# Kernel tuning notes

Hardware: AMD Instinct MI355X
Metric: run time of the kernel (lower is better)

Reference implementation:

```python
import jax, jax.numpy as jnp
import numpy as np

B = 32768
H = 320          # pred_hidden
V = 34           # num_classes
BLANK = V - 1    # padding_idx for embedding


def setup_inputs() -> dict:
    key = jax.random.key(0)
    ks = jax.random.split(key, 12)
    s = 0.05
    embed_W = jax.random.normal(ks[0], (V, H), jnp.float32) * s
    embed_W = embed_W.at[BLANK].set(0.0)  # padding_idx row is zeros in torch
    return {
        "x": jax.random.randint(ks[1], (B,), 0, V, jnp.int32),
        "enc_proj_line": jax.random.normal(ks[2], (B, H), jnp.float32),
        "h": jax.random.normal(ks[3], (1, B, H), jnp.float32),
        "c": jax.random.normal(ks[4], (1, B, H), jnp.float32),
        "embed_W": embed_W,
        "W_ih": jax.random.normal(ks[5], (4 * H, H), jnp.float32) * s,
        "W_hh": jax.random.normal(ks[6], (4 * H, H), jnp.float32) * s,
        "b_ih": jax.random.normal(ks[7], (4 * H,), jnp.float32) * s,
        "b_hh": jax.random.normal(ks[8], (4 * H,), jnp.float32) * s,
        "pred_W": jax.random.normal(ks[9], (H, H), jnp.float32) * s,
        "pred_b": jnp.zeros((H,), jnp.float32),
        "joint_W": jax.random.normal(ks[10], (V, H), jnp.float32) * s,
        "joint_b": jnp.zeros((V,), jnp.float32),
    }


def reference(x, enc_proj_line, h, c, embed_W, W_ih, W_hh, b_ih, b_hh,
              pred_W, pred_b, joint_W, joint_b):
    # embedding lookup: [B, H]
    emb = embed_W[x]
    # single-timestep LSTM cell (torch gate order: i, f, g, o)
    gates = emb @ W_ih.T + b_ih + h[0] @ W_hh.T + b_hh  # [B, 4H]
    i, f, g, o = jnp.split(gates, 4, axis=-1)
    i = jax.nn.sigmoid(i)
    f = jax.nn.sigmoid(f)
    g = jnp.tanh(g)
    o = jax.nn.sigmoid(o)
    c_new = f * c[0] + i * g                 # [B, H]
    h_new = o * jnp.tanh(c_new)              # [B, H] == g[0] (lstm output)
    # pred projection + joint
    pred_proj = h_new @ pred_W.T + pred_b    # [B, H]
    joint_out = (enc_proj_line + pred_proj) @ joint_W.T + joint_b  # [B, V]
    dec = jnp.argmax(joint_out, axis=-1)
    return dec, h_new[None], c_new[None]
```

## Files before the change

### kernel.cpp

```cpp
#include <hip/hip_runtime.h>
#include <math.h>

#define NB 32768
#define H 320
#define V 34
#define N4 1280
#define BM 128
#define BN 128
#define KSTEPS 10
#define NWIN 5
#define NWG ((NB / BM) * (N4 / BN))

typedef _Float16 f16;
typedef f16 f16x4 __attribute__((ext_vector_type(4)));
typedef f16 f16x8 __attribute__((ext_vector_type(8)));
typedef float f32x4 __attribute__((ext_vector_type(4)));

#define WS_GTP 0
#define WS_JB2 54400
#define WS_B_BYTE 217744
#define BT_COUNT (N4 * H)
#define WS_JP_BYTE 1856144
#define JP_COUNT (48 * 640)
#define WS_AT_BYTE 1979136
#define AT_COUNT (NB * H)

#define JBM 64
#define JBK 32
#define JKSTEPS 20

#define PREP_P4 1280
#define PREP_P2 50
#define PREP_P0 170
#define PREP_P3 120
#define PREP_NWG (PREP_P4 + PREP_P2 + PREP_P0 + PREP_P3 + 1)

__device__ __forceinline__ float sigf(float x) {
    return 1.0f / (1.0f + __expf(-x));
}
__device__ __forceinline__ float tanh_fast(float x) {
    return 1.0f - 2.0f / (1.0f + __expf(2.0f * x));
}

typedef const __attribute__((address_space(1))) unsigned int* gas_t;
typedef __attribute__((address_space(3))) unsigned int* las_t;

__device__ __forceinline__ void split8(const float* e, f16x8& p1, f16x8& p2) {
    #pragma unroll
    for (int j = 0; j < 8; ++j) {
        f16 a = (f16)e[j];
        p1[j] = a;
        p2[j] = (f16)((e[j] - (float)a) * 2048.0f);
    }
}

__device__ __forceinline__ void split8_res(const float* e, f16x8& p1, f16x8& p2) {
    #pragma unroll
    for (int j = 0; j < 8; ++j) {
        f16 a = (f16)e[j];
        p1[j] = a;
        p2[j] = (f16)(e[j] - (float)a);
    }
}

__global__ void prep(const float* __restrict__ embed_W,
                     const float* __restrict__ W_ih,
                     const float* __restrict__ b_ih,
                     const float* __restrict__ b_hh,
                     const float* __restrict__ pred_W,
                     const float* __restrict__ pred_b,
                     const float* __restrict__ joint_W,
                     const float* __restrict__ joint_b,
                     const float* __restrict__ W_hh,
                     const float* __restrict__ h_in,
                     float* __restrict__ ws) {
    const int bid = blockIdx.x;
    const int t = threadIdx.x;
    if (bid < PREP_P4) {
        int id = bid * 256 + t;
        int ks = id >> 15, m = id & 32767;
        const float* src = h_in + (size_t)m * H + ks * 32;
        f16* at1 = (f16*)((char*)ws + WS_AT_BYTE);
        f16* at2 = at1 + AT_COUNT;
        size_t tbase = ((size_t)(m >> 7) * KSTEPS + ks) * 4096
                       + ((m & 127) >> 4) * 512 + (m & 15) * 8;
        #pragma unroll
        for (int g = 0; g < 4; ++g) {
            float4 v0 = *(const float4*)(src + g * 8);
            float4 v1 = *(const float4*)(src + g * 8 + 4);
            float e[8] = {v0.x, v0.y, v0.z, v0.w, v1.x, v1.y, v1.z, v1.w};
            f16x8 p1, p2;
            split8_res(e, p1, p2);
            *(f16x8*)(at1 + tbase + g * 128) = p1;
            *(f16x8*)(at2 + tbase + g * 128) = p2;
        }
    } else if (bid < PREP_P4 + PREP_P2) {
        int id = (bid - PREP_P4) * 256 + t;
        int ks = id / 1280, n = id - ks * 1280;
        int orig = (n & 3) * H + (n >> 2);
        const float* src = W_hh + (size_t)orig * H + ks * 32;
        f16* bt1 = (f16*)((char*)ws + WS_B_BYTE);
        f16* bt2 = bt1 + BT_COUNT;
        size_t tbase = ((size_t)(n >> 7) * KSTEPS + ks) * 4096
                       + ((n & 127) >> 4) * 512 + (n & 15) * 8;
        #pragma unroll
        for (int g = 0; g < 4; ++g) {
            float4 v0 = *(const float4*)(src + g * 8);
            float4 v1 = *(const float4*)(src + g * 8 + 4);
            float e[8] = {v0.x, v0.y, v0.z, v0.w, v1.x, v1.y, v1.z, v1.w};
            f16x8 p1, p2;
            split8(e, p1, p2);
            *(f16x8*)(bt1 + tbase + g * 128) = p1;
            *(f16x8*)(bt2 + tbase + g * 128) = p2;
        }
    } else if (bid < PREP_P4 + PREP_P2 + PREP_P0) {
        int id = (bid - PREP_P4 - PREP_P2) * 256 + t;
        int v = id / N4, n = id % N4;
        int orig = (n & 3) * H + (n >> 2);
        float acc = b_ih[orig] + b_hh[orig];
        const float* e = embed_W + (size_t)v * H;
        const float* w = W_ih + (size_t)orig * H;
        for (int k = 0; k < H; k += 4) {
            float4 e4 = *(const float4*)(e + k);
            float4 w4 = *(const float4*)(w + k);
            acc = fmaf(e4.x, w4.x, acc);
            acc = fmaf(e4.y, w4.y, acc);
            acc = fmaf(e4.z, w4.z, acc);
            acc = fmaf(e4.w, w4.w, acc);
        }
        ws[WS_GTP + id] = acc;
    } else if (bid < PREP_P4 + PREP_P2 + PREP_P0 + PREP_P3) {
        int id = (bid - PREP_P4 - PREP_P2 - PREP_P0) * 256 + t;
        int n = id / 640, k = id % 640;
        float wv = 0.0f;
        if (n < V) {
            if (k < H) {
                wv = joint_W[(size_t)n * H + k];
            } else {
                float acc = 0.0f;
                const float* jw = joint_W + (size_t)n * H;
                for (int j = 0; j < H; ++j)
                    acc = fmaf(jw[j], pred_W[(size_t)j * H + (k - H)], acc);
                wv = acc;
            }
        }
        f16 w1 = (f16)wv;
        f16 w2 = (f16)((wv - (float)w1) * 2048.0f);
        int kk = k & 31;
        int off = (k >> 5) * 1536 + (n >> 4) * 512 + (kk >> 3) * 128
                  + (n & 15) * 8 + (kk & 7);
        f16* jp1 = (f16*)((char*)ws + WS_JP_BYTE);
        jp1[off] = w1;
        jp1[JP_COUNT + off] = w2;
    } else {
        if (t < V) {
            float acc = joint_b[t];
            const float* jw = joint_W + (size_t)t * H;
            for (int j = 0; j < H; ++j)
                acc = fmaf(jw[j], pred_b[j], acc);
            ws[WS_JB2 + t] = acc;
        }
    }
}

__launch_bounds__(256, 2)
__global__ void lstm_gemm_fast(const int* __restrict__ x,
                               const float* __restrict__ c_in,
                               const float* __restrict__ ws,
                               float* __restrict__ out) {
    __shared__ __align__(16) char smem[65536];
    const int tid = threadIdx.x, lane = tid & 63, w = tid >> 6;

    int l = (blockIdx.x & 7) * (NWG / 8) + (blockIdx.x >> 3);
    const int mb = l / (N4 / BN);
    const int nb = l % (N4 / BN);
    const int m0 = mb * BM, n0 = nb * BN;

    const f16* At1 = (const f16*)((const char*)ws + WS_AT_BYTE);
    const f16* At2 = At1 + AT_COUNT;
    const f16* Bt1 = (const f16*)((const char*)ws + WS_B_BYTE);
    const f16* Bt2 = Bt1 + BT_COUNT;
    const float* gtp = ws + WS_GTP;
    float* hn_out = out + NB;
    float* cn_out = out + NB + (size_t)NB * H;

    const int asub = (w >> 1) * 4;
    const int bsub = (w & 1) * 4;
    const int lo = lane * 8;

    auto stageB = [&](int T, int parity) {
        const f16* srcp = (w < 2) ? Bt1 : Bt2;
        const int p = (w < 2) ? 0 : 1;
        #pragma unroll
        for (int ksl = 0; ksl < 2; ++ksl) {
            const f16* src = srcp + (size_t)(nb * KSTEPS + 2 * T + ksl) * 4096
                             + (w & 1) * 2048;
            char* dst = smem + parity * 32768 + p * 16384 + ksl * 8192
                        + (w & 1) * 4096;
            #pragma unroll
            for (int i = 0; i < 4; ++i) {
                __builtin_amdgcn_global_load_lds(
                    (gas_t)(const void*)(src + i * 512 + lane * 8),
                    (las_t)(void*)(dst + i * 1024), 16, 0, 0);
            }
        }
    };

    f32x4 acc[4][4];
    #pragma unroll
    for (int i = 0; i < 4; ++i)
        #pragma unroll
        for (int j = 0; j < 4; ++j)
            acc[i][j] = (f32x4){0.f, 0.f, 0.f, 0.f};

    stageB(0, 0);
    __syncthreads();

    const int hk0 = n0 >> 2;
    float cpre[16];
    #pragma unroll
    for (int it = 0; it < 16; ++it)
        cpre[it] = c_in[(size_t)(m0 + it * 8 + (tid >> 5)) * H + hk0 + (tid & 31)];

    #pragma unroll
    for (int T = 0; T < NWIN; ++T) {
        const int par = T & 1;
        const f16* B1 = (const f16*)(smem + par * 32768);
        const f16* B2 = B1 + 8192;

        f16x8 b1a[4], b2a[4];
        #pragma unroll
        for (int nj = 0; nj < 4; ++nj) {
            b1a[nj] = *(const f16x8*)(B1 + (bsub + nj) * 512 + lo);
            b2a[nj] = *(const f16x8*)(B2 + (bsub + nj) * 512 + lo);
        }
        f16x8 a1a[4], a2a[4];
        {
            const f16* a1b = At1 + (size_t)(mb * KSTEPS + 2 * T) * 4096;
            const f16* a2b = At2 + (size_t)(mb * KSTEPS + 2 * T) * 4096;
            #pragma unroll
            for (int mi = 0; mi < 4; ++mi) {
                a1a[mi] = *(const f16x8*)(a1b + (asub + mi) * 512 + lo);
                a2a[mi] = *(const f16x8*)(a2b + (asub + mi) * 512 + lo);
            }
        }
        if (T < NWIN - 1) stageB(T + 1, par ^ 1);

        __builtin_amdgcn_s_setprio(1);
        #pragma unroll
        for (int mi = 0; mi < 4; ++mi)
            #pragma unroll
            for (int nj = 0; nj < 4; ++nj)
                acc[mi][nj] = __builtin_amdgcn_mfma_f32_16x16x32_f16(
                    a1a[mi], b1a[nj], acc[mi][nj], 0, 0, 0);
        __builtin_amdgcn_s_setprio(0);
        #pragma unroll
        for (int mi = 0; mi < 4; ++mi)
            #pragma unroll
            for (int j = 0; j < 8; ++j)
                a1a[mi][j] = a1a[mi][j] * (f16)0.00048828125f;
        __builtin_amdgcn_s_setprio(1);
        #pragma unroll
        for (int mi = 0; mi < 4; ++mi)
            #pragma unroll
            for (int nj = 0; nj < 4; ++nj)
                acc[mi][nj] = __builtin_amdgcn_mfma_f32_16x16x32_f16(
                    a1a[mi], b2a[nj], acc[mi][nj], 0, 0, 0);
        __builtin_amdgcn_s_setprio(0);

        f16x8 a1c[4], a2c[4];
        {
            const f16* a1b = At1 + (size_t)(mb * KSTEPS + 2 * T + 1) * 4096;
            const f16* a2b = At2 + (size_t)(mb * KSTEPS + 2 * T + 1) * 4096;
            #pragma unroll
            for (int mi = 0; mi < 4; ++mi) {
                a1c[mi] = *(const f16x8*)(a1b + (asub + mi) * 512 + lo);
                a2c[mi] = *(const f16x8*)(a2b + (asub + mi) * 512 + lo);
            }
        }

        __builtin_amdgcn_s_setprio(1);
        #pragma unroll
        for (int mi = 0; mi < 4; ++mi)
            #pragma unroll
            for (int nj = 0; nj < 4; ++nj)
                acc[mi][nj] = __builtin_amdgcn_mfma_f32_16x16x32_f16(
                    a2a[mi], b1a[nj], acc[mi][nj], 0, 0, 0);
        __builtin_amdgcn_s_setprio(0);

        f16x8 b1c[4], b2c[4];
        #pragma unroll
        for (int nj = 0; nj < 4; ++nj) {
            b1c[nj] = *(const f16x8*)(B1 + 4096 + (bsub + nj) * 512 + lo);
            b2c[nj] = *(const f16x8*)(B2 + 4096 + (bsub + nj) * 512 + lo);
        }
        __builtin_amdgcn_s_setprio(1);
        #pragma unroll
        for (int mi = 0; mi < 4; ++mi)
            #pragma unroll
            for (int nj = 0; nj < 4; ++nj)
                acc[mi][nj] = __builtin_amdgcn_mfma_f32_16x16x32_f16(
                    a1c[mi], b1c[nj], acc[mi][nj], 0, 0, 0);
        __builtin_amdgcn_s_setprio(0);
        #pragma unroll
        for (int mi = 0; mi < 4; ++mi)
            #pragma unroll
            for (int j = 0; j < 8; ++j)
                a1c[mi][j] = a1c[mi][j] * (f16)0.00048828125f;
        __builtin_amdgcn_s_setprio(1);
        #pragma unroll
        for (int mi = 0; mi < 4; ++mi)
            #pragma unroll
            for (int nj = 0; nj < 4; ++nj)
                acc[mi][nj] = __builtin_amdgcn_mfma_f32_16x16x32_f16(
                    a1c[mi], b2c[nj], acc[mi][nj], 0, 0, 0);
        #pragma unroll
        for (int mi = 0; mi < 4; ++mi)
            #pragma unroll
            for (int nj = 0; nj < 4; ++nj)
                acc[mi][nj] = __builtin_amdgcn_mfma_f32_16x16x32_f16(
                    a2c[mi], b1c[nj], acc[mi][nj], 0, 0, 0);
        __builtin_amdgcn_s_setprio(0);

        __syncthreads();
    }

    const int wm = (w >> 1) * 64, wn = (w & 1) * 64;
    float* gates = (float*)smem;
    #pragma unroll
    for (int mi = 0; mi < 4; ++mi)
        #pragma unroll
        for (int nj = 0; nj < 4; ++nj) {
            f32x4 v = acc[mi][nj];
            int n = wn + nj * 16 + (lane & 15);
            int r0 = wm + mi * 16 + (lane >> 4) * 4;
            #pragma unroll
            for (int q = 0; q < 4; ++q) {
                int row = r0 + q;
                gates[row * 128 + (n ^ ((row & 7) << 2))] = v[q];
            }
        }
    __syncthreads();

    #pragma unroll
    for (int it = 0; it < 16; ++it) {
        int ml = it * 8 + (tid >> 5), hkl = tid & 31;
        int k0s = (ml & 7) << 2;
        f32x4 g4 = *(const f32x4*)&gates[ml * 128 + ((hkl * 4) ^ k0s)];
        int m = m0 + ml;
        int hk = hk0 + hkl;
        int xv = x[m];
        float4 b4 = *(const float4*)(gtp + (size_t)xv * N4 + n0 + hkl * 4);
        float ig = sigf(g4[0] + b4.x);
        float fg = sigf(g4[1] + b4.y);
        float gg = tanh_fast(g4[2] + b4.z);
        float og = sigf(g4[3] + b4.w);
        float cn = fmaf(fg, cpre[it], ig * gg);
        float hn = og * tanh_fast(cn);
        hn_out[(size_t)m * H + hk] = hn;
        cn_out[(size_t)m * H + hk] = cn;
    }
}

__launch_bounds__(256, 2)
__global__ void joint_argmax(const float* __restrict__ enc,
                             const float* __restrict__ ws,
                             float* __restrict__ out) {
    __shared__ __align__(16) char smem[28672];
    const int tid = threadIdx.x, lane = tid & 63, w = tid >> 6;
    const int m0 = blockIdx.x * JBM;

    const f16* Jp1 = (const f16*)((const char*)ws + WS_JP_BYTE);
    const f16* Jp2 = Jp1 + JP_COUNT;
    const float* hn = out + NB;
    const float* jb2 = ws + WS_JB2;

    f16* base = (f16*)smem;

    f32x4 accM[3], accC[3];
    #pragma unroll
    for (int j = 0; j < 3; ++j) {
        accM[j] = (f32x4){0.f, 0.f, 0.f, 0.f};
        accC[j] = (f32x4){0.f, 0.f, 0.f, 0.f};
    }

    auto stage = [&](int t, f16* A1, f16* A2, f16* B1, f16* B2) {
        const float* srcp = (t < 10) ? enc : hn;
        const int koff = (t % 10) * JBK;
        int row = (tid >> 6) * 16 + (tid & 15);
        int k0 = ((tid & 63) >> 4) * 8;
        const float* sp = srcp + (size_t)(m0 + row) * H + koff + k0;
        float4 v0 = *(const float4*)sp;
        float4 v1 = *(const float4*)(sp + 4);
        float e[8] = {v0.x, v0.y, v0.z, v0.w, v1.x, v1.y, v1.z, v1.w};
        f16x8 p1, p2;
        split8(e, p1, p2);
        *(f16x8*)(A1 + tid * 8) = p1;
        *(f16x8*)(A2 + tid * 8) = p2;
        if (tid < 192) {
            *(int4*)(B1 + tid * 8) = *(const int4*)(Jp1 + t * 1536 + tid * 8);
            *(int4*)(B2 + tid * 8) = *(const int4*)(Jp2 + t * 1536 + tid * 8);
        }
    };

    stage(0, base, base + 2048, base + 4096, base + 5632);
    __syncthreads();

    const int lo = lane * 8;
    int cur = 0;
    for (int t = 0; t < JKSTEPS; ++t) {
        if (t < JKSTEPS - 1) {
            f16* nb_ = base + (cur ^ 1) * 7168;
            stage(t + 1, nb_, nb_ + 2048, nb_ + 4096, nb_ + 5632);
        }
        f16* A1 = base + cur * 7168;
        f16* A2 = A1 + 2048;
        f16* B1 = A1 + 4096;
        f16* B2 = A1 + 5632;

        f16x8 a1 = *(const f16x8*)(A1 + w * 512 + lo);
        f16x8 a2 = *(const f16x8*)(A2 + w * 512 + lo);
        f16x8 b1[3], b2[3];
        #pragma unroll
        for (int nj = 0; nj < 3; ++nj) {
            b1[nj] = *(const f16x8*)(B1 + nj * 512 + lo);
            b2[nj] = *(const f16x8*)(B2 + nj * 512 + lo);
        }
        #pragma unroll
        for (int nj = 0; nj < 3; ++nj) {
            accM[nj] = __builtin_amdgcn_mfma_f32_16x16x32_f16(a1, b1[nj], accM[nj], 0, 0, 0);
            accC[nj] = __builtin_amdgcn_mfma_f32_16x16x32_f16(a1, b2[nj], accC[nj], 0, 0, 0);
            accC[nj] = __builtin_amdgcn_mfma_f32_16x16x32_f16(a2, b1[nj], accC[nj], 0, 0, 0);
        }
        __syncthreads();
        cur ^= 1;
    }

    float* lg = (float*)smem;
    const int wm = w * 16;
    #pragma unroll
    for (int nj = 0; nj < 3; ++nj) {
        int n = nj * 16 + (lane & 15);
        int mr = wm + (lane >> 4) * 4;
        #pragma unroll
        for (int q = 0; q < 4; ++q)
            lg[(mr + q) * 49 + n] = fmaf(accC[nj][q], 1.0f / 2048.0f, accM[nj][q]);
    }
    __syncthreads();

    if (tid < JBM) {
        const float* row = lg + tid * 49;
        float best = row[0] + jb2[0];
        int bi = 0;
        #pragma unroll
        for (int v = 1; v < V; ++v) {
            float t2 = row[v] + jb2[v];
            if (t2 > best) { best = t2; bi = v; }
        }
        out[m0 + tid] = (float)bi;
    }
}

extern "C" void kernel_launch(void* const* d_in, const int* in_sizes, int n_in,
                              void* d_out, int out_size, void* d_ws, size_t ws_size,
                              hipStream_t stream) {
    const int*   x       = (const int*)  d_in[0];
    const float* enc     = (const float*)d_in[1];
    const float* h       = (const float*)d_in[2];
    const float* c       = (const float*)d_in[3];
    const float* embed_W = (const float*)d_in[4];
    const float* W_ih    = (const float*)d_in[5];
    const float* W_hh    = (const float*)d_in[6];
    const float* b_ih    = (const float*)d_in[7];
    const float* b_hh    = (const float*)d_in[8];
    const float* pred_W  = (const float*)d_in[9];
    const float* pred_b  = (const float*)d_in[10];
    const float* joint_W = (const float*)d_in[11];
    const float* joint_b = (const float*)d_in[12];
    float* out = (float*)d_out;
    float* ws  = (float*)d_ws;

    prep<<<PREP_NWG, 256, 0, stream>>>(embed_W, W_ih, b_ih, b_hh,
                                       pred_W, pred_b, joint_W, joint_b,
                                       W_hh, h, ws);
    lstm_gemm_fast<<<NWG, 256, 0, stream>>>(x, c, ws, out);
    joint_argmax<<<NB / JBM, 256, 0, stream>>>(enc, ws, out);
}
```

Baseline: 159.6 us.

## Fuse h fp16 split conversion into LSTM GEMM, drop prep tiling pass

Removes the prep stage that converted the fp32 hidden state into two tiled fp16 hi/lo arrays in workspace. The GEMM kernel now loads fp32 h rows directly and performs the hi/lo split in registers right before the MFMAs. This removes a large workspace write and readback. In exchange, conversion is repeated per N-block and the loads are less coalesced than the pre-tiled layout.

```diff
diff --git a/kernel.cpp b/kernel.cpp
--- a/kernel.cpp
+++ b/kernel.cpp
@@ -22,18 +22,15 @@
 #define BT_COUNT (N4 * H)
 #define WS_JP_BYTE 1856144
 #define JP_COUNT (48 * 640)
-#define WS_AT_BYTE 1979136
-#define AT_COUNT (NB * H)
 
 #define JBM 64
 #define JBK 32
 #define JKSTEPS 20
 
-#define PREP_P4 1280
 #define PREP_P2 50
 #define PREP_P0 170
 #define PREP_P3 120
-#define PREP_NWG (PREP_P4 + PREP_P2 + PREP_P0 + PREP_P3 + 1)
+#define PREP_NWG (PREP_P2 + PREP_P0 + PREP_P3 + 1)
 
 __device__ __forceinline__ float sigf(float x) {
     return 1.0f / (1.0f + __expf(-x));
@@ -54,7 +51,9 @@
     }
 }
 
-__device__ __forceinline__ void split8_res(const float* e, f16x8& p1, f16x8& p2) {
+__device__ __forceinline__ void cvt_split(const float4& v0, const float4& v1,
+                                          f16x8& p1, f16x8& p2) {
+    float e[8] = {v0.x, v0.y, v0.z, v0.w, v1.x, v1.y, v1.z, v1.w};
     #pragma unroll
     for (int j = 0; j < 8; ++j) {
         f16 a = (f16)e[j];
@@ -72,30 +71,11 @@
                      const float* __restrict__ joint_W,
                      const float* __restrict__ joint_b,
                      const float* __restrict__ W_hh,
-                     const float* __restrict__ h_in,
                      float* __restrict__ ws) {
     const int bid = blockIdx.x;
     const int t = threadIdx.x;
-    if (bid < PREP_P4) {
+    if (bid < PREP_P2) {
         int id = bid * 256 + t;
-        int ks = id >> 15, m = id & 32767;
-        const float* src = h_in + (size_t)m * H + ks * 32;
-        f16* at1 = (f16*)((char*)ws + WS_AT_BYTE);
-        f16* at2 = at1 + AT_COUNT;
-        size_t tbase = ((size_t)(m >> 7) * KSTEPS + ks) * 4096
-                       + ((m & 127) >> 4) * 512 + (m & 15) * 8;
-        #pragma unroll
-        for (int g = 0; g < 4; ++g) {
-            float4 v0 = *(const float4*)(src + g * 8);
-            float4 v1 = *(const float4*)(src + g * 8 + 4);
-            float e[8] = {v0.x, v0.y, v0.z, v0.w, v1.x, v1.y, v1.z, v1.w};
-            f16x8 p1, p2;
-            split8_res(e, p1, p2);
-            *(f16x8*)(at1 + tbase + g * 128) = p1;
-            *(f16x8*)(at2 + tbase + g * 128) = p2;
-        }
-    } else if (bid < PREP_P4 + PREP_P2) {
-        int id = (bid - PREP_P4) * 256 + t;
         int ks = id / 1280, n = id - ks * 1280;
         int orig = (n & 3) * H + (n >> 2);
         const float* src = W_hh + (size_t)orig * H + ks * 32;
@@ -113,8 +93,8 @@
             *(f16x8*)(bt1 + tbase + g * 128) = p1;
             *(f16x8*)(bt2 + tbase + g * 128) = p2;
         }
-    } else if (bid < PREP_P4 + PREP_P2 + PREP_P0) {
-        int id = (bid - PREP_P4 - PREP_P2) * 256 + t;
+    } else if (bid < PREP_P2 + PREP_P0) {
+        int id = (bid - PREP_P2) * 256 + t;
         int v = id / N4, n = id % N4;
         int orig = (n & 3) * H + (n >> 2);
         float acc = b_ih[orig] + b_hh[orig];
@@ -129,8 +109,8 @@
             acc = fmaf(e4.w, w4.w, acc);
         }
         ws[WS_GTP + id] = acc;
-    } else if (bid < PREP_P4 + PREP_P2 + PREP_P0 + PREP_P3) {
-        int id = (bid - PREP_P4 - PREP_P2 - PREP_P0) * 256 + t;
+    } else if (bid < PREP_P2 + PREP_P0 + PREP_P3) {
+        int id = (bid - PREP_P2 - PREP_P0) * 256 + t;
         int n = id / 640, k = id % 640;
         float wv = 0.0f;
         if (n < V) {
@@ -165,6 +145,7 @@
 
 __launch_bounds__(256, 2)
 __global__ void lstm_gemm_fast(const int* __restrict__ x,
+                               const float* __restrict__ h_in,
                                const float* __restrict__ c_in,
                                const float* __restrict__ ws,
                                float* __restrict__ out) {
@@ -176,8 +157,6 @@
     const int nb = l % (N4 / BN);
     const int m0 = mb * BM, n0 = nb * BN;
 
-    const f16* At1 = (const f16*)((const char*)ws + WS_AT_BYTE);
-    const f16* At2 = At1 + AT_COUNT;
     const f16* Bt1 = (const f16*)((const char*)ws + WS_B_BYTE);
     const f16* Bt2 = Bt1 + BT_COUNT;
     const float* gtp = ws + WS_GTP;
@@ -188,6 +167,12 @@
     const int bsub = (w & 1) * 4;
     const int lo = lane * 8;
 
+    const float* hrow[4];
+    #pragma unroll
+    for (int mi = 0; mi < 4; ++mi)
+        hrow[mi] = h_in + (size_t)(m0 + (asub + mi) * 16 + (lane & 15)) * H
+                   + (lane >> 4) * 8;
+
     auto stageB = [&](int T, int parity) {
         const f16* srcp = (w < 2) ? Bt1 : Bt2;
         const int p = (w < 2) ? 0 : 1;
@@ -234,17 +219,18 @@
             b1a[nj] = *(const f16x8*)(B1 + (bsub + nj) * 512 + lo);
             b2a[nj] = *(const f16x8*)(B2 + (bsub + nj) * 512 + lo);
         }
+        float4 av0[4], av1[4];
+        #pragma unroll
+        for (int mi = 0; mi < 4; ++mi) {
+            av0[mi] = *(const float4*)(hrow[mi] + (2 * T) * 32);
+            av1[mi] = *(const float4*)(hrow[mi] + (2 * T) * 32 + 4);
+        }
+        if (T < NWIN - 1) stageB(T + 1, par ^ 1);
+
         f16x8 a1a[4], a2a[4];
-        {
-            const f16* a1b = At1 + (size_t)(mb * KSTEPS + 2 * T) * 4096;
-            const f16* a2b = At2 + (size_t)(mb * KSTEPS + 2 * T) * 4096;
-            #pragma unroll
-            for (int mi = 0; mi < 4; ++mi) {
-                a1a[mi] = *(const f16x8*)(a1b + (asub + mi) * 512 + lo);
-                a2a[mi] = *(const f16x8*)(a2b + (asub + mi) * 512 + lo);
-            }
-        }
-        if (T < NWIN - 1) stageB(T + 1, par ^ 1);
+        #pragma unroll
+        for (int mi = 0; mi < 4; ++mi)
+            cvt_split(av0[mi], av1[mi], a1a[mi], a2a[mi]);
 
         __builtin_amdgcn_s_setprio(1);
         #pragma unroll
@@ -259,6 +245,12 @@
             #pragma unroll
             for (int j = 0; j < 8; ++j)
                 a1a[mi][j] = a1a[mi][j] * (f16)0.00048828125f;
+        float4 cv0[4], cv1[4];
+        #pragma unroll
+        for (int mi = 0; mi < 4; ++mi) {
+            cv0[mi] = *(const float4*)(hrow[mi] + (2 * T + 1) * 32);
+            cv1[mi] = *(const float4*)(hrow[mi] + (2 * T + 1) * 32 + 4);
+        }
         __builtin_amdgcn_s_setprio(1);
         #pragma unroll
         for (int mi = 0; mi < 4; ++mi)
@@ -266,20 +258,6 @@
             for (int nj = 0; nj < 4; ++nj)
                 acc[mi][nj] = __builtin_amdgcn_mfma_f32_16x16x32_f16(
                     a1a[mi], b2a[nj], acc[mi][nj], 0, 0, 0);
-        __builtin_amdgcn_s_setprio(0);
-
-        f16x8 a1c[4], a2c[4];
-        {
-            const f16* a1b = At1 + (size_t)(mb * KSTEPS + 2 * T + 1) * 4096;
-            const f16* a2b = At2 + (size_t)(mb * KSTEPS + 2 * T + 1) * 4096;
-            #pragma unroll
-            for (int mi = 0; mi < 4; ++mi) {
-                a1c[mi] = *(const f16x8*)(a1b + (asub + mi) * 512 + lo);
-                a2c[mi] = *(const f16x8*)(a2b + (asub + mi) * 512 + lo);
-            }
-        }
-
-        __builtin_amdgcn_s_setprio(1);
         #pragma unroll
         for (int mi = 0; mi < 4; ++mi)
             #pragma unroll
@@ -294,6 +272,11 @@
             b1c[nj] = *(const f16x8*)(B1 + 4096 + (bsub + nj) * 512 + lo);
             b2c[nj] = *(const f16x8*)(B2 + 4096 + (bsub + nj) * 512 + lo);
         }
+        f16x8 a1c[4], a2c[4];
+        #pragma unroll
+        for (int mi = 0; mi < 4; ++mi)
+            cvt_split(cv0[mi], cv1[mi], a1c[mi], a2c[mi]);
+
         __builtin_amdgcn_s_setprio(1);
         #pragma unroll
         for (int mi = 0; mi < 4; ++mi)
@@ -482,7 +465,7 @@
 
     prep<<<PREP_NWG, 256, 0, stream>>>(embed_W, W_ih, b_ih, b_hh,
                                        pred_W, pred_b, joint_W, joint_b,
-                                       W_hh, h, ws);
-    lstm_gemm_fast<<<NWG, 256, 0, stream>>>(x, c, ws, out);
+                                       W_hh, ws);
+    lstm_gemm_fast<<<NWG, 256, 0, stream>>>(x, h, c, ws, out);
     joint_argmax<<<NB / JBM, 256, 0, stream>>>(enc, ws, out);
 }
```

New measurement: 196.3 us. +22.9%, slower.
